# Performance work log

Hardware: AMD Instinct MI355X
Metric: run time of the kernel (lower is better)

Reference implementation:

```python
import jax, jax.numpy as jnp
import numpy as np

DT = 0.1
GRAVITY = 9.81
DENSITY = 1028.0
ZVEC = jnp.array([0.0, 0.0, 1.0], dtype=jnp.float32)


def _skew(v):
    # v: [k,3] -> [k,3,3] skew-symmetric matrix (matches A/B/C column construction)
    x, y, z = v[..., 0], v[..., 1], v[..., 2]
    o = jnp.zeros_like(x)
    r0 = jnp.stack([o, -z, y], -1)
    r1 = jnp.stack([z, o, -x], -1)
    r2 = jnp.stack([-y, x, o], -1)
    return jnp.stack([r0, r1, r2], -2)


def _body2inertial(pose):
    # pose: [k,7]; quat stored as (x,y,z,w) in pose[:,3:7]
    q = pose[:, 3:7]
    x, y, z, w = q[:, 0], q[:, 1], q[:, 2], q[:, 3]
    r0 = jnp.stack([1 - 2 * (y * y + z * z), 2 * (x * y - z * w), 2 * (x * z + y * w)], -1)
    r1 = jnp.stack([2 * (x * y + z * w), 1 - 2 * (x * x + z * z), 2 * (y * z - x * w)], -1)
    r2 = jnp.stack([2 * (x * z - y * w), 2 * (y * z + x * w), 1 - 2 * (x * x + y * y)], -1)
    rot = jnp.stack([r0, r1, r2], -2)  # [k,3,3]
    t = 0.5 * jnp.stack([
        jnp.stack([-x, -y, -z], -1),
        jnp.stack([w, -z, y], -1),
        jnp.stack([z, w, -x], -1),
        jnp.stack([-y, x, w], -1)], -2)  # [k,4,3]
    return rot, t


def _restoring(rot, mass, volume, cog, cob):
    fng = -mass * GRAVITY * ZVEC              # (3,)
    fnb = volume * DENSITY * GRAVITY * ZVEC   # (3,)
    # rotItoB = rot^T -> rot^T @ f == einsum('kji,j->ki')
    fbg = jnp.einsum('kji,j->ki', rot, fng)
    fbb = jnp.einsum('kji,j->ki', rot, fnb)
    mbg = jnp.cross(cog, fbg)
    mbb = jnp.cross(cob, fbb)
    return -jnp.concatenate([fbg + fbb, mbg + mbb], -1)  # [k,6]


def _damping(v, linDamp, linDampFow, quadDamp):
    eye6 = jnp.eye(6, dtype=v.dtype)
    D = -linDamp - v[:, :, None] * linDampFow
    return D - quadDamp * (jnp.abs(v)[:, :, None] * eye6)  # [k,6,6]


def _coriolis(v, mTot):
    M = mTot[0]
    mv_top = jnp.einsum('ij,kj->ki', M[0:3, 0:3], v[:, 0:3]) + jnp.einsum('ij,kj->ki', M[0:3, 3:6], v[:, 3:6])
    mv_bot = jnp.einsum('ij,kj->ki', M[3:6, 0:3], v[:, 0:3]) + jnp.einsum('ij,kj->ki', M[3:6, 3:6], v[:, 3:6])
    s12 = -_skew(mv_top)
    s22 = -_skew(mv_bot)
    z33 = jnp.zeros_like(s12)
    r1 = jnp.concatenate([z33, s12], -1)
    r2 = jnp.concatenate([s12, s22], -1)  # note: source uses s12 (not s12^T) in lower-left, reproduced faithfully
    return jnp.concatenate([r1, r2], -2)  # [k,6,6]


def _dot(x, u, mass, volume, cog, cob, mTot, linDamp, linDampFow, quadDamp):
    p, v = x[:, 0:7], x[:, 7:13]
    rot, t = _body2inertial(p)
    # jacobian is block-diag [[rot,0],[0,t]] -> apply blocks directly
    pDot_lin = jnp.einsum('kij,kj->ki', rot, v[:, 0:3])  # [k,3]
    pDot_ang = jnp.einsum('kij,kj->ki', t, v[:, 3:6])    # [k,4]
    D = _damping(v, linDamp, linDampFow, quadDamp)
    C = _coriolis(v, mTot)
    Dv = jnp.einsum('kij,kj->ki', D, v)
    Cv = jnp.einsum('kij,kj->ki', C, v)
    g = _restoring(rot, mass, volume, cog, cob)
    rhs = u - Cv - Dv - g                      # [k,6]
    vDot = jnp.linalg.solve(mTot[0], rhs.T).T  # single shared 6x6 solve
    return jnp.concatenate([pDot_lin, pDot_ang, vDot], -1)  # [k,13]


def _norm_quat(xs):
    q = xs[:, 3:7]
    q = q / jnp.linalg.norm(q, axis=-1, keepdims=True)
    return xs.at[:, 3:7].set(q)


def reference(x, u, mass, volume, cog, cob, mTot, linDamp, linDampFow, quadDamp):
    # RK2 integration step (rk=2 default)
    k1 = _dot(x, u, mass, volume, cog, cob, mTot, linDamp, linDampFow, quadDamp)
    k2 = _dot(x + k1 * DT, u, mass, volume, cog, cob, mTot, linDamp, linDampFow, quadDamp)
    return _norm_quat(x + (DT / 2.0) * (k1 + k2))


def setup_inputs() -> dict:
    key = jax.random.key(0)
    kx, ku = jax.random.split(key)
    K = 524288
    x = jax.random.normal(kx, (K, 13), dtype=jnp.float32)
    u = jax.random.normal(ku, (K, 6), dtype=jnp.float32)
    mass = jnp.array([100.0], dtype=jnp.float32)
    volume = jnp.array([1.0], dtype=jnp.float32)
    cog = jnp.zeros((1, 3), dtype=jnp.float32)
    cob = jnp.array([[0.0, 0.0, 0.2]], dtype=jnp.float32)
    rb = np.zeros((6, 6), dtype=np.float32)
    rb[0:3, 0:3] = 100.0 * np.eye(3, dtype=np.float32)
    ma = 100.0 * np.eye(6, dtype=np.float32) + 1e-7      # default Ma (+1e-7 on every entry)
    mTot = jnp.asarray(rb + ma)[None]                    # [1,6,6]
    linDamp = jnp.diag(jnp.array([-70.0, -70.0, -700.0, -300.0, -300.0, -100.0], dtype=jnp.float32))[None]
    linDampFow = jnp.zeros((1, 6, 6), dtype=jnp.float32)
    quadDamp = jnp.diag(jnp.array([-740.0, -990.0, -1800.0, -670.0, -770.0, -520.0], dtype=jnp.float32))[None]
    return {"x": x, "u": u, "mass": mass, "volume": volume, "cog": cog, "cob": cob,
            "mTot": mTot, "linDamp": linDamp, "linDampFow": linDampFow, "quadDamp": quadDamp}
```

## Files before the change

### kernel.cpp

```cpp
#include <hip/hip_runtime.h>
#include <math.h>


__device__ __forceinline__ float fast_rcp(float x) {
    float r = __builtin_amdgcn_rcpf(x);
    return r * (2.0f - x * r);
}

__device__ __forceinline__ void fossen_dot(const float* __restrict__ X,
                                           const float* __restrict__ U,
                                           const float* __restrict__ smi,
                                           const float* __restrict__ mTot,
                                           const float* __restrict__ linDamp,
                                           const float* __restrict__ linDampFow,
                                           const float* __restrict__ qdiag,
                                           const float* __restrict__ lddiag,
                                           const float* __restrict__ cgcb,
                                           float fgz, float fbz,
                                           bool ldDiag, bool ldfZero,
                                           float* __restrict__ xd)
{
    const float qx = X[3], qy = X[4], qz = X[5], qw = X[6];
    const float r00 = 1.f - 2.f*(qy*qy + qz*qz);
    const float r01 = 2.f*(qx*qy - qz*qw);
    const float r02 = 2.f*(qx*qz + qy*qw);
    const float r10 = 2.f*(qx*qy + qz*qw);
    const float r11 = 1.f - 2.f*(qx*qx + qz*qz);
    const float r12 = 2.f*(qy*qz - qx*qw);
    const float r20 = 2.f*(qx*qz - qy*qw);
    const float r21 = 2.f*(qy*qz + qx*qw);
    const float r22 = 1.f - 2.f*(qx*qx + qy*qy);

    const float v0 = X[7],  v1 = X[8],  v2 = X[9];
    const float v3 = X[10], v4 = X[11], v5 = X[12];

    xd[0] = r00*v0 + r01*v1 + r02*v2;
    xd[1] = r10*v0 + r11*v1 + r12*v2;
    xd[2] = r20*v0 + r21*v1 + r22*v2;
    xd[3] = 0.5f*(-qx*v3 - qy*v4 - qz*v5);
    xd[4] = 0.5f*( qw*v3 - qz*v4 + qy*v5);
    xd[5] = 0.5f*( qz*v3 + qw*v4 - qx*v5);
    xd[6] = 0.5f*(-qy*v3 + qx*v4 + qw*v5);

    const float v[6] = {v0, v1, v2, v3, v4, v5};

    float P[6];
#pragma unroll
    for (int i = 0; i < 6; ++i)
        P[i] = lddiag[i]*v[i] + qdiag[i]*fabsf(v[i])*v[i];
    if (!ldDiag) {
#pragma unroll
        for (int i = 0; i < 6; ++i) {
            float ld = 0.f;
#pragma unroll
            for (int j = 0; j < 6; ++j)
                if (j != i) ld += linDamp[i*6 + j] * v[j];
            P[i] += ld;
        }
    }
    if (!ldfZero) {
#pragma unroll
        for (int i = 0; i < 6; ++i) {
            float ldf = 0.f;
#pragma unroll
            for (int j = 0; j < 6; ++j) ldf += linDampFow[i*6 + j] * v[j];
            P[i] += v[i]*ldf;
        }
    }

    float mv[6];
#pragma unroll
    for (int i = 0; i < 6; ++i) {
        float s = 0.f;
#pragma unroll
        for (int j = 0; j < 6; ++j) s += mTot[i*6 + j] * v[j];
        mv[i] = s;
    }
    float Cv[6];
    Cv[0] = -(mv[1]*v5 - mv[2]*v4);
    Cv[1] = -(mv[2]*v3 - mv[0]*v5);
    Cv[2] = -(mv[0]*v4 - mv[1]*v3);
    Cv[3] = -(mv[1]*v2 - mv[2]*v1) - (mv[4]*v5 - mv[5]*v4);
    Cv[4] = -(mv[2]*v0 - mv[0]*v2) - (mv[5]*v3 - mv[3]*v5);
    Cv[5] = -(mv[0]*v1 - mv[1]*v0) - (mv[3]*v4 - mv[4]*v3);

    const float fb0 = r20*fgz, fb1 = r21*fgz, fb2 = r22*fgz;
    const float bb0 = r20*fbz, bb1 = r21*fbz, bb2 = r22*fbz;
    const float cgx = cgcb[0], cgy = cgcb[1], cgz = cgcb[2];
    const float cbx = cgcb[3], cby = cgcb[4], cbz = cgcb[5];
    const float m0 = cgy*fb2 - cgz*fb1 + cby*bb2 - cbz*bb1;
    const float m1 = cgz*fb0 - cgx*fb2 + cbz*bb0 - cbx*bb2;
    const float m2 = cgx*fb1 - cgy*fb0 + cbx*bb1 - cby*bb0;
    const float g[6] = { -(fb0+bb0), -(fb1+bb1), -(fb2+bb2), -m0, -m1, -m2 };

    float rhs[6];
#pragma unroll
    for (int i = 0; i < 6; ++i) rhs[i] = U[i] - Cv[i] + P[i] - g[i];

#pragma unroll
    for (int i = 0; i < 6; ++i) {
        const float4 m4 = *(const float4*)(&smi[i*8]);
        const float2 m2 = *(const float2*)(&smi[i*8 + 4]);
        xd[7+i] = m4.x*rhs[0] + m4.y*rhs[1] + m4.z*rhs[2] + m4.w*rhs[3]
                + m2.x*rhs[4] + m2.y*rhs[5];
    }
}

__device__ __forceinline__ void gj_inverse_to_lds(const float* __restrict__ mTot,
                                                  float* __restrict__ smiw)
{
    float a[36], Mi[36];
#pragma unroll
    for (int i = 0; i < 36; ++i) a[i] = mTot[i];
#pragma unroll
    for (int i = 0; i < 36; ++i) Mi[i] = 0.f;
#pragma unroll
    for (int i = 0; i < 6; ++i) Mi[i*6 + i] = 1.f;
#pragma unroll
    for (int col = 0; col < 6; ++col) {
        const float d = fast_rcp(a[col*6 + col]);
#pragma unroll
        for (int j = 0; j < 6; ++j) { a[col*6+j] *= d; Mi[col*6+j] *= d; }
#pragma unroll
        for (int r = 0; r < 6; ++r) {
            if (r == col) continue;
            const float f = a[r*6 + col];
#pragma unroll
            for (int j = 0; j < 6; ++j) {
                a[r*6+j]  -= f * a[col*6+j];
                Mi[r*6+j] -= f * Mi[col*6+j];
            }
        }
    }
#pragma unroll
    for (int r = 0; r < 6; ++r)
#pragma unroll
        for (int c = 0; c < 6; ++c) smiw[r*8 + c] = Mi[r*6 + c];
}

__global__ void __launch_bounds__(256, 4)
auv_rk2_fused(const float* __restrict__ x, const float* __restrict__ u,
              const float* __restrict__ mass, const float* __restrict__ volume,
              const float* __restrict__ cog, const float* __restrict__ cob,
              const float* __restrict__ mTot, const float* __restrict__ linDamp,
              const float* __restrict__ linDampFow,
              const float* __restrict__ quadDamp,
              float* __restrict__ out, int K)
{
    __shared__ float sx[256 * 13];
    __shared__ float smi[4][48];
    const int tid   = threadIdx.x;
    const int w     = tid >> 6;
    const int l     = tid & 63;
    const int wf4   = w * 208;
    const int base  = blockIdx.x * 256;
    const int nElem = min(256, K - base);

    float qdiag[6], lddiag[6], cgcb[6];
#pragma unroll
    for (int i = 0; i < 6; ++i) { qdiag[i] = quadDamp[i*6+i]; lddiag[i] = linDamp[i*6+i]; }
#pragma unroll
    for (int i = 0; i < 3; ++i) { cgcb[i] = cog[i]; cgcb[3+i] = cob[i]; }
    const float fgz = -mass[0] * 9.81f;
    const float fbz =  volume[0] * 1028.0f * 9.81f;

    bool ldDiag = true, ldfZero = true;
#pragma unroll
    for (int i = 0; i < 6; ++i)
#pragma unroll
        for (int j = 0; j < 6; ++j) {
            ldfZero = ldfZero && (linDampFow[i*6+j] == 0.0f);
            if (i != j) ldDiag = ldDiag && (linDamp[i*6+j] == 0.0f);
        }

    if (nElem == 256) {
        const float* gx = x + (size_t)base * 13;
#pragma unroll
        for (int it = 0; it < 3; ++it) {
            const int k = wf4 + it*64 + l;
            __builtin_amdgcn_global_load_lds(
                (const __attribute__((address_space(1))) void*)(gx + (size_t)k*4),
                (__attribute__((address_space(3))) void*)(&sx[k*4]), 16, 0, 0);
        }
        if (l < 16) {
            const int k = wf4 + 192 + l;
            __builtin_amdgcn_global_load_lds(
                (const __attribute__((address_space(1))) void*)(gx + (size_t)k*4),
                (__attribute__((address_space(3))) void*)(&sx[k*4]), 16, 0, 0);
        }

        float U[6];
        {
            const float* gu = u + (size_t)(base + tid) * 6;
            const float2 a2 = *(const float2*)(gu);
            const float2 b2 = *(const float2*)(gu + 2);
            const float2 c2 = *(const float2*)(gu + 4);
            U[0]=a2.x; U[1]=a2.y; U[2]=b2.x; U[3]=b2.y; U[4]=c2.x; U[5]=c2.y;
        }

        if (l == 0) gj_inverse_to_lds(mTot, &smi[w][0]);

        asm volatile("s_waitcnt vmcnt(0) lgkmcnt(0)" ::: "memory");

        float X[13];
#pragma unroll
        for (int j = 0; j < 13; ++j) X[j] = sx[tid*13 + j];

        float k1[13], X2[13], k2[13], Y[13];
        fossen_dot(X, U, &smi[w][0], mTot, linDamp, linDampFow, qdiag, lddiag,
                   cgcb, fgz, fbz, ldDiag, ldfZero, k1);
#pragma unroll
        for (int j = 0; j < 13; ++j) X2[j] = X[j] + 0.1f * k1[j];
        fossen_dot(X2, U, &smi[w][0], mTot, linDamp, linDampFow, qdiag, lddiag,
                   cgcb, fgz, fbz, ldDiag, ldfZero, k2);
#pragma unroll
        for (int j = 0; j < 13; ++j) Y[j] = X[j] + 0.05f * (k1[j] + k2[j]);

        const float nq  = Y[3]*Y[3] + Y[4]*Y[4] + Y[5]*Y[5] + Y[6]*Y[6];
        float inv = __builtin_amdgcn_rsqf(nq);
        inv = inv * (1.5f - 0.5f * nq * inv * inv);
        Y[3] *= inv; Y[4] *= inv; Y[5] *= inv; Y[6] *= inv;

#pragma unroll
        for (int j = 0; j < 13; ++j) sx[tid*13 + j] = Y[j];

        asm volatile("s_waitcnt lgkmcnt(0)" ::: "memory");

        float4*       go = (float4*)(out + (size_t)base * 13);
        const float4* s4 = (const float4*)sx;
#pragma unroll
        for (int it = 0; it < 3; ++it) {
            const int k = wf4 + it*64 + l;
            go[k] = s4[k];
        }
        if (l < 16) {
            const int k = wf4 + 192 + l;
            go[k] = s4[k];
        }
    } else {
        for (int k = tid; k < nElem*13; k += 256) sx[k] = x[(size_t)base*13 + k];

        float U[6] = {0,0,0,0,0,0};
        if (tid < nElem) {
            const float* gu = u + (size_t)(base + tid) * 6;
            const float2 a2 = *(const float2*)(gu);
            const float2 b2 = *(const float2*)(gu + 2);
            const float2 c2 = *(const float2*)(gu + 4);
            U[0]=a2.x; U[1]=a2.y; U[2]=b2.x; U[3]=b2.y; U[4]=c2.x; U[5]=c2.y;
        }
        if (tid == 0) gj_inverse_to_lds(mTot, &smi[0][0]);
        __syncthreads();

        if (tid < nElem) {
            float X[13];
#pragma unroll
            for (int j = 0; j < 13; ++j) X[j] = sx[tid*13 + j];

            float k1[13], X2[13], k2[13], Y[13];
            fossen_dot(X, U, &smi[0][0], mTot, linDamp, linDampFow, qdiag,
                       lddiag, cgcb, fgz, fbz, ldDiag, ldfZero, k1);
#pragma unroll
            for (int j = 0; j < 13; ++j) X2[j] = X[j] + 0.1f * k1[j];
            fossen_dot(X2, U, &smi[0][0], mTot, linDamp, linDampFow, qdiag,
                       lddiag, cgcb, fgz, fbz, ldDiag, ldfZero, k2);
#pragma unroll
            for (int j = 0; j < 13; ++j) Y[j] = X[j] + 0.05f * (k1[j] + k2[j]);

            const float nq  = Y[3]*Y[3] + Y[4]*Y[4] + Y[5]*Y[5] + Y[6]*Y[6];
            float inv = __builtin_amdgcn_rsqf(nq);
            inv = inv * (1.5f - 0.5f * nq * inv * inv);
            Y[3] *= inv; Y[4] *= inv; Y[5] *= inv; Y[6] *= inv;
#pragma unroll
            for (int j = 0; j < 13; ++j) sx[tid*13 + j] = Y[j];
        }
        __syncthreads();
        for (int k = tid; k < nElem*13; k += 256) out[(size_t)base*13 + k] = sx[k];
    }
}

extern "C" void kernel_launch(void* const* d_in, const int* in_sizes, int n_in,
                              void* d_out, int out_size, void* d_ws, size_t ws_size,
                              hipStream_t stream)
{
    const float* x          = (const float*)d_in[0];
    const float* u          = (const float*)d_in[1];
    const float* mass       = (const float*)d_in[2];
    const float* volume     = (const float*)d_in[3];
    const float* cog        = (const float*)d_in[4];
    const float* cob        = (const float*)d_in[5];
    const float* mTot       = (const float*)d_in[6];
    const float* linDamp    = (const float*)d_in[7];
    const float* linDampFow = (const float*)d_in[8];
    const float* quadDamp   = (const float*)d_in[9];
    float*       out        = (float*)d_out;

    const int K = in_sizes[0] / 13;
    const int blocks = (K + 255) / 256;
    auv_rk2_fused<<<blocks, 256, 0, stream>>>(x, u, mass, volume, cog, cob,
                                              mTot, linDamp, linDampFow,
                                              quadDamp, out, K);
}
```

Measured before the change: 118.7 us.

## Process two element tiles per block, pipelining async LDS loads with compute

Each 256-thread block now handles 512 elements in two halves. Both halves' x and u data are issued up front as async global-to-LDS loads, with u now staged through LDS instead of per-thread float2 loads. Partial vmcnt waits let the first half's compute overlap the second half's loads, and each half's output is stored before the next half is computed. LDS use per block roughly triples, which may limit how many blocks fit per CU, and the grid has half as many blocks.

Measured after the change: 120.7 us. Within noise of the previous version (+1.7%).

```diff
diff --git a/kernel.cpp b/kernel.cpp
--- a/kernel.cpp
+++ b/kernel.cpp
@@ -147,14 +147,14 @@
               const float* __restrict__ quadDamp,
               float* __restrict__ out, int K)
 {
-    __shared__ float sx[256 * 13];
+    __shared__ float sx[512 * 13];
+    __shared__ float su[512 * 6];
     __shared__ float smi[4][48];
     const int tid   = threadIdx.x;
     const int w     = tid >> 6;
     const int l     = tid & 63;
-    const int wf4   = w * 208;
-    const int base  = blockIdx.x * 256;
-    const int nElem = min(256, K - base);
+    const int base  = blockIdx.x * 512;
+    const int nElem = min(512, K - base);
 
     float qdiag[6], lddiag[6], cgcb[6];
 #pragma unroll
@@ -173,95 +173,69 @@
             if (i != j) ldDiag = ldDiag && (linDamp[i*6+j] == 0.0f);
         }
 
-    if (nElem == 256) {
+    if (nElem == 512) {
         const float* gx = x + (size_t)base * 13;
-#pragma unroll
-        for (int it = 0; it < 3; ++it) {
-            const int k = wf4 + it*64 + l;
-            __builtin_amdgcn_global_load_lds(
-                (const __attribute__((address_space(1))) void*)(gx + (size_t)k*4),
-                (__attribute__((address_space(3))) void*)(&sx[k*4]), 16, 0, 0);
-        }
-        if (l < 16) {
-            const int k = wf4 + 192 + l;
-            __builtin_amdgcn_global_load_lds(
-                (const __attribute__((address_space(1))) void*)(gx + (size_t)k*4),
-                (__attribute__((address_space(3))) void*)(&sx[k*4]), 16, 0, 0);
-        }
-
-        float U[6];
-        {
-            const float* gu = u + (size_t)(base + tid) * 6;
-            const float2 a2 = *(const float2*)(gu);
-            const float2 b2 = *(const float2*)(gu + 2);
-            const float2 c2 = *(const float2*)(gu + 4);
-            U[0]=a2.x; U[1]=a2.y; U[2]=b2.x; U[3]=b2.y; U[4]=c2.x; U[5]=c2.y;
+        const float* gu = u + (size_t)base * 6;
+
+#pragma unroll
+        for (int t = 0; t < 2; ++t) {
+            const int xb = t*832 + w*208;
+#pragma unroll
+            for (int it = 0; it < 3; ++it) {
+                const int k = xb + it*64 + l;
+                __builtin_amdgcn_global_load_lds(
+                    (const __attribute__((address_space(1))) void*)(gx + (size_t)k*4),
+                    (__attribute__((address_space(3))) void*)(&sx[k*4]), 16, 0, 0);
+            }
+            if (l < 16) {
+                const int k = xb + 192 + l;
+                __builtin_amdgcn_global_load_lds(
+                    (const __attribute__((address_space(1))) void*)(gx + (size_t)k*4),
+                    (__attribute__((address_space(3))) void*)(&sx[k*4]), 16, 0, 0);
+            }
+            const int ub = t*384 + w*96;
+            {
+                const int k = ub + l;
+                __builtin_amdgcn_global_load_lds(
+                    (const __attribute__((address_space(1))) void*)(gu + (size_t)k*4),
+                    (__attribute__((address_space(3))) void*)(&su[k*4]), 16, 0, 0);
+            }
+            if (l < 32) {
+                const int k = ub + 64 + l;
+                __builtin_amdgcn_global_load_lds(
+                    (const __attribute__((address_space(1))) void*)(gu + (size_t)k*4),
+                    (__attribute__((address_space(3))) void*)(&su[k*4]), 16, 0, 0);
+            }
         }
 
         if (l == 0) gj_inverse_to_lds(mTot, &smi[w][0]);
-
-        asm volatile("s_waitcnt vmcnt(0) lgkmcnt(0)" ::: "memory");
-
-        float X[13];
-#pragma unroll
-        for (int j = 0; j < 13; ++j) X[j] = sx[tid*13 + j];
-
-        float k1[13], X2[13], k2[13], Y[13];
-        fossen_dot(X, U, &smi[w][0], mTot, linDamp, linDampFow, qdiag, lddiag,
-                   cgcb, fgz, fbz, ldDiag, ldfZero, k1);
-#pragma unroll
-        for (int j = 0; j < 13; ++j) X2[j] = X[j] + 0.1f * k1[j];
-        fossen_dot(X2, U, &smi[w][0], mTot, linDamp, linDampFow, qdiag, lddiag,
-                   cgcb, fgz, fbz, ldDiag, ldfZero, k2);
-#pragma unroll
-        for (int j = 0; j < 13; ++j) Y[j] = X[j] + 0.05f * (k1[j] + k2[j]);
-
-        const float nq  = Y[3]*Y[3] + Y[4]*Y[4] + Y[5]*Y[5] + Y[6]*Y[6];
-        float inv = __builtin_amdgcn_rsqf(nq);
-        inv = inv * (1.5f - 0.5f * nq * inv * inv);
-        Y[3] *= inv; Y[4] *= inv; Y[5] *= inv; Y[6] *= inv;
-
-#pragma unroll
-        for (int j = 0; j < 13; ++j) sx[tid*13 + j] = Y[j];
-
-        asm volatile("s_waitcnt lgkmcnt(0)" ::: "memory");
 
         float4*       go = (float4*)(out + (size_t)base * 13);
         const float4* s4 = (const float4*)sx;
-#pragma unroll
-        for (int it = 0; it < 3; ++it) {
-            const int k = wf4 + it*64 + l;
-            go[k] = s4[k];
-        }
-        if (l < 16) {
-            const int k = wf4 + 192 + l;
-            go[k] = s4[k];
-        }
-    } else {
-        for (int k = tid; k < nElem*13; k += 256) sx[k] = x[(size_t)base*13 + k];
-
-        float U[6] = {0,0,0,0,0,0};
-        if (tid < nElem) {
-            const float* gu = u + (size_t)(base + tid) * 6;
-            const float2 a2 = *(const float2*)(gu);
-            const float2 b2 = *(const float2*)(gu + 2);
-            const float2 c2 = *(const float2*)(gu + 4);
-            U[0]=a2.x; U[1]=a2.y; U[2]=b2.x; U[3]=b2.y; U[4]=c2.x; U[5]=c2.y;
-        }
-        if (tid == 0) gj_inverse_to_lds(mTot, &smi[0][0]);
-        __syncthreads();
-
-        if (tid < nElem) {
-            float X[13];
-#pragma unroll
-            for (int j = 0; j < 13; ++j) X[j] = sx[tid*13 + j];
+
+#pragma unroll
+        for (int t = 0; t < 2; ++t) {
+            if (t == 0) {
+                asm volatile("s_waitcnt vmcnt(6) lgkmcnt(0)" ::: "memory");
+            } else {
+                asm volatile("s_waitcnt vmcnt(4)" ::: "memory");
+            }
+            __builtin_amdgcn_sched_barrier(0);
+
+            const int rowf = t*3328 + tid*13;
+            const int uf   = t*1536 + tid*6;
+            float X[13], U[6];
+#pragma unroll
+            for (int j = 0; j < 13; ++j) X[j] = sx[rowf + j];
+#pragma unroll
+            for (int j = 0; j < 6; ++j)  U[j] = su[uf + j];
 
             float k1[13], X2[13], k2[13], Y[13];
-            fossen_dot(X, U, &smi[0][0], mTot, linDamp, linDampFow, qdiag,
+            fossen_dot(X, U, &smi[w][0], mTot, linDamp, linDampFow, qdiag,
                        lddiag, cgcb, fgz, fbz, ldDiag, ldfZero, k1);
 #pragma unroll
             for (int j = 0; j < 13; ++j) X2[j] = X[j] + 0.1f * k1[j];
-            fossen_dot(X2, U, &smi[0][0], mTot, linDamp, linDampFow, qdiag,
+            fossen_dot(X2, U, &smi[w][0], mTot, linDamp, linDampFow, qdiag,
                        lddiag, cgcb, fgz, fbz, ldDiag, ldfZero, k2);
 #pragma unroll
             for (int j = 0; j < 13; ++j) Y[j] = X[j] + 0.05f * (k1[j] + k2[j]);
@@ -270,8 +244,57 @@
             float inv = __builtin_amdgcn_rsqf(nq);
             inv = inv * (1.5f - 0.5f * nq * inv * inv);
             Y[3] *= inv; Y[4] *= inv; Y[5] *= inv; Y[6] *= inv;
-#pragma unroll
-            for (int j = 0; j < 13; ++j) sx[tid*13 + j] = Y[j];
+
+#pragma unroll
+            for (int j = 0; j < 13; ++j) sx[rowf + j] = Y[j];
+
+            asm volatile("s_waitcnt lgkmcnt(0)" ::: "memory");
+            __builtin_amdgcn_sched_barrier(0);
+
+            const int xb = t*832 + w*208;
+#pragma unroll
+            for (int it = 0; it < 3; ++it) {
+                const int k = xb + it*64 + l;
+                go[k] = s4[k];
+            }
+            if (l < 16) {
+                const int k = xb + 192 + l;
+                go[k] = s4[k];
+            }
+        }
+    } else {
+        for (int k = tid; k < nElem*13; k += 256) sx[k] = x[(size_t)base*13 + k];
+        if (tid == 0) gj_inverse_to_lds(mTot, &smi[0][0]);
+        __syncthreads();
+
+#pragma unroll
+        for (int rr = 0; rr < 2; ++rr) {
+            const int r = tid + rr*256;
+            if (r < nElem) {
+                float X[13], U[6];
+#pragma unroll
+                for (int j = 0; j < 13; ++j) X[j] = sx[r*13 + j];
+                const float* gu = u + (size_t)(base + r) * 6;
+#pragma unroll
+                for (int j = 0; j < 6; ++j) U[j] = gu[j];
+
+                float k1[13], X2[13], k2[13], Y[13];
+                fossen_dot(X, U, &smi[0][0], mTot, linDamp, linDampFow, qdiag,
+                           lddiag, cgcb, fgz, fbz, ldDiag, ldfZero, k1);
+#pragma unroll
+                for (int j = 0; j < 13; ++j) X2[j] = X[j] + 0.1f * k1[j];
+                fossen_dot(X2, U, &smi[0][0], mTot, linDamp, linDampFow, qdiag,
+                           lddiag, cgcb, fgz, fbz, ldDiag, ldfZero, k2);
+#pragma unroll
+                for (int j = 0; j < 13; ++j) Y[j] = X[j] + 0.05f * (k1[j] + k2[j]);
+
+                const float nq  = Y[3]*Y[3] + Y[4]*Y[4] + Y[5]*Y[5] + Y[6]*Y[6];
+                float inv = __builtin_amdgcn_rsqf(nq);
+                inv = inv * (1.5f - 0.5f * nq * inv * inv);
+                Y[3] *= inv; Y[4] *= inv; Y[5] *= inv; Y[6] *= inv;
+#pragma unroll
+                for (int j = 0; j < 13; ++j) sx[r*13 + j] = Y[j];
+            }
         }
         __syncthreads();
         for (int k = tid; k < nElem*13; k += 256) out[(size_t)base*13 + k] = sx[k];
@@ -295,7 +318,7 @@
     float*       out        = (float*)d_out;
 
     const int K = in_sizes[0] / 13;
-    const int blocks = (K + 255) / 256;
+    const int blocks = (K + 511) / 512;
     auv_rk2_fused<<<blocks, 256, 0, stream>>>(x, u, mass, volume, cog, cob,
                                               mTot, linDamp, linDampFow,
                                               quadDamp, out, K);
```

## Load and store state directly per thread, dropping LDS staging of x and output

Applied to the files above, without the earlier changes.

Replaces the LDS-staged coalesced load/store of the 13-float state (global_load_lds plus float4 copy-out) with per-thread unaligned vector loads and stores straight from and to global memory. This removes the LDS buffer, the round trips through LDS and the separate tail-block path, and it also frees shared memory for occupancy. The trade-off is a 52-byte per-thread stride, so global accesses become less coalesced and some vector accesses are misaligned.

After: 116.4 us. -2.0%, faster.

```diff
diff --git a/kernel.cpp b/kernel.cpp
--- a/kernel.cpp
+++ b/kernel.cpp
@@ -1,6 +1,9 @@
 #include <hip/hip_runtime.h>
 #include <math.h>
 
+
+typedef float f4u __attribute__((ext_vector_type(4), aligned(4)));
+typedef float f2u __attribute__((ext_vector_type(2), aligned(8)));
 
 __device__ __forceinline__ float fast_rcp(float x) {
     float r = __builtin_amdgcn_rcpf(x);
@@ -147,14 +150,27 @@
               const float* __restrict__ quadDamp,
               float* __restrict__ out, int K)
 {
-    __shared__ float sx[256 * 13];
     __shared__ float smi[4][48];
-    const int tid   = threadIdx.x;
-    const int w     = tid >> 6;
-    const int l     = tid & 63;
-    const int wf4   = w * 208;
-    const int base  = blockIdx.x * 256;
-    const int nElem = min(256, K - base);
+    const int tid = threadIdx.x;
+    const int w   = tid >> 6;
+    const int l   = tid & 63;
+    const int idx = blockIdx.x * 256 + tid;
+    const bool live = (idx < K);
+
+    f4u xa = {0,0,0,0}, xb = {0,0,0,0}, xc = {0,0,0,0};
+    float xd13 = 0.f;
+    f2u ua = {0,0}, ub = {0,0}, uc = {0,0};
+    if (live) {
+        const float* gxr = x + (size_t)idx * 13;
+        xa = *(const f4u*)(gxr);
+        xb = *(const f4u*)(gxr + 4);
+        xc = *(const f4u*)(gxr + 8);
+        xd13 = gxr[12];
+        const float* gur = u + (size_t)idx * 6;
+        ua = *(const f2u*)(gur);
+        ub = *(const f2u*)(gur + 2);
+        uc = *(const f2u*)(gur + 4);
+    }
 
     float qdiag[6], lddiag[6], cgcb[6];
 #pragma unroll
@@ -173,38 +189,17 @@
             if (i != j) ldDiag = ldDiag && (linDamp[i*6+j] == 0.0f);
         }
 
-    if (nElem == 256) {
-        const float* gx = x + (size_t)base * 13;
-#pragma unroll
-        for (int it = 0; it < 3; ++it) {
-            const int k = wf4 + it*64 + l;
-            __builtin_amdgcn_global_load_lds(
-                (const __attribute__((address_space(1))) void*)(gx + (size_t)k*4),
-                (__attribute__((address_space(3))) void*)(&sx[k*4]), 16, 0, 0);
-        }
-        if (l < 16) {
-            const int k = wf4 + 192 + l;
-            __builtin_amdgcn_global_load_lds(
-                (const __attribute__((address_space(1))) void*)(gx + (size_t)k*4),
-                (__attribute__((address_space(3))) void*)(&sx[k*4]), 16, 0, 0);
-        }
-
-        float U[6];
-        {
-            const float* gu = u + (size_t)(base + tid) * 6;
-            const float2 a2 = *(const float2*)(gu);
-            const float2 b2 = *(const float2*)(gu + 2);
-            const float2 c2 = *(const float2*)(gu + 4);
-            U[0]=a2.x; U[1]=a2.y; U[2]=b2.x; U[3]=b2.y; U[4]=c2.x; U[5]=c2.y;
-        }
-
-        if (l == 0) gj_inverse_to_lds(mTot, &smi[w][0]);
-
-        asm volatile("s_waitcnt vmcnt(0) lgkmcnt(0)" ::: "memory");
-
-        float X[13];
-#pragma unroll
-        for (int j = 0; j < 13; ++j) X[j] = sx[tid*13 + j];
+    if (l == 0) gj_inverse_to_lds(mTot, &smi[w][0]);
+    asm volatile("s_waitcnt lgkmcnt(0)" ::: "memory");
+    __builtin_amdgcn_sched_barrier(0);
+
+    if (live) {
+        float X[13], U[6];
+        X[0]=xa.x;  X[1]=xa.y;  X[2]=xa.z;  X[3]=xa.w;
+        X[4]=xb.x;  X[5]=xb.y;  X[6]=xb.z;  X[7]=xb.w;
+        X[8]=xc.x;  X[9]=xc.y;  X[10]=xc.z; X[11]=xc.w;
+        X[12]=xd13;
+        U[0]=ua.x; U[1]=ua.y; U[2]=ub.x; U[3]=ub.y; U[4]=uc.x; U[5]=uc.y;
 
         float k1[13], X2[13], k2[13], Y[13];
         fossen_dot(X, U, &smi[w][0], mTot, linDamp, linDampFow, qdiag, lddiag,
@@ -221,60 +216,15 @@
         inv = inv * (1.5f - 0.5f * nq * inv * inv);
         Y[3] *= inv; Y[4] *= inv; Y[5] *= inv; Y[6] *= inv;
 
-#pragma unroll
-        for (int j = 0; j < 13; ++j) sx[tid*13 + j] = Y[j];
-
-        asm volatile("s_waitcnt lgkmcnt(0)" ::: "memory");
-
-        float4*       go = (float4*)(out + (size_t)base * 13);
-        const float4* s4 = (const float4*)sx;
-#pragma unroll
-        for (int it = 0; it < 3; ++it) {
-            const int k = wf4 + it*64 + l;
-            go[k] = s4[k];
-        }
-        if (l < 16) {
-            const int k = wf4 + 192 + l;
-            go[k] = s4[k];
-        }
-    } else {
-        for (int k = tid; k < nElem*13; k += 256) sx[k] = x[(size_t)base*13 + k];
-
-        float U[6] = {0,0,0,0,0,0};
-        if (tid < nElem) {
-            const float* gu = u + (size_t)(base + tid) * 6;
-            const float2 a2 = *(const float2*)(gu);
-            const float2 b2 = *(const float2*)(gu + 2);
-            const float2 c2 = *(const float2*)(gu + 4);
-            U[0]=a2.x; U[1]=a2.y; U[2]=b2.x; U[3]=b2.y; U[4]=c2.x; U[5]=c2.y;
-        }
-        if (tid == 0) gj_inverse_to_lds(mTot, &smi[0][0]);
-        __syncthreads();
-
-        if (tid < nElem) {
-            float X[13];
-#pragma unroll
-            for (int j = 0; j < 13; ++j) X[j] = sx[tid*13 + j];
-
-            float k1[13], X2[13], k2[13], Y[13];
-            fossen_dot(X, U, &smi[0][0], mTot, linDamp, linDampFow, qdiag,
-                       lddiag, cgcb, fgz, fbz, ldDiag, ldfZero, k1);
-#pragma unroll
-            for (int j = 0; j < 13; ++j) X2[j] = X[j] + 0.1f * k1[j];
-            fossen_dot(X2, U, &smi[0][0], mTot, linDamp, linDampFow, qdiag,
-                       lddiag, cgcb, fgz, fbz, ldDiag, ldfZero, k2);
-#pragma unroll
-            for (int j = 0; j < 13; ++j) Y[j] = X[j] + 0.05f * (k1[j] + k2[j]);
-
-            const float nq  = Y[3]*Y[3] + Y[4]*Y[4] + Y[5]*Y[5] + Y[6]*Y[6];
-            float inv = __builtin_amdgcn_rsqf(nq);
-            inv = inv * (1.5f - 0.5f * nq * inv * inv);
-            Y[3] *= inv; Y[4] *= inv; Y[5] *= inv; Y[6] *= inv;
-#pragma unroll
-            for (int j = 0; j < 13; ++j) sx[tid*13 + j] = Y[j];
-        }
-        __syncthreads();
-        for (int k = tid; k < nElem*13; k += 256) out[(size_t)base*13 + k] = sx[k];
+        float* gor = out + (size_t)idx * 13;
+        f4u ya, yb, yc;
+        ya.x=Y[0];  ya.y=Y[1];  ya.z=Y[2];  ya.w=Y[3];
+        yb.x=Y[4];  yb.y=Y[5];  yb.z=Y[6];  yb.w=Y[7];
+        yc.x=Y[8];  yc.y=Y[9];  yc.z=Y[10]; yc.w=Y[11];
+        *(f4u*)(gor)     = ya;
+        *(f4u*)(gor + 4) = yb;
+        *(f4u*)(gor + 8) = yc;
+        gor[12] = Y[12];
     }
 }
 
```
